# Kernel optimization log

Hardware: AMD Instinct MI355X
Metric: run time of the kernel (lower is better)

The kernel has to match this reference:

```python
import jax, jax.numpy as jnp
import numpy as np

B, CD, GD, F, H = 8192, 512, 512, 1024, 8
HD = F // H
EPS = 1e-5  # torch LayerNorm default


def _layernorm(x, g, b):
    m = x.mean(-1, keepdims=True)
    v = ((x - m) ** 2).mean(-1, keepdims=True)
    return (x - m) / jnp.sqrt(v + EPS) * g + b


def setup_inputs() -> dict:
    key = jax.random.key(0)
    ks = jax.random.split(key, 24)
    s = lambda fan_in: 1.0 / np.sqrt(fan_in)
    return {
        "cnn_embed": jax.random.normal(ks[0], (B, CD), jnp.float32),
        "gnn_embed": jax.random.normal(ks[1], (B, GD), jnp.float32),
        # projections (torch Linear: y = x @ W.T + b)
        "cnn_w": jax.random.normal(ks[2], (F, CD), jnp.float32) * s(CD),
        "cnn_b": jax.random.normal(ks[3], (F,), jnp.float32) * s(CD),
        "gnn_w": jax.random.normal(ks[4], (F, GD), jnp.float32) * s(GD),
        "gnn_b": jax.random.normal(ks[5], (F,), jnp.float32) * s(GD),
        # layernorms
        "ln1_g": jnp.ones((F,), jnp.float32),
        "ln1_b": jnp.zeros((F,), jnp.float32),
        "ln2_g": jnp.ones((F,), jnp.float32),
        "ln2_b": jnp.zeros((F,), jnp.float32),
        # MultiheadAttention packed in-proj + out-proj
        "attn_in_w": jax.random.normal(ks[6], (3 * F, F), jnp.float32) * s(F),
        "attn_in_b": jnp.zeros((3 * F,), jnp.float32),
        "attn_out_w": jax.random.normal(ks[7], (F, F), jnp.float32) * s(F),
        "attn_out_b": jnp.zeros((F,), jnp.float32),
        # gate MLP: Linear(2F->F) GELU Linear(F->2) Softmax
        "gate_w1": jax.random.normal(ks[8], (F, 2 * F), jnp.float32) * s(2 * F),
        "gate_b1": jnp.zeros((F,), jnp.float32),
        "gate_w2": jax.random.normal(ks[9], (2, F), jnp.float32) * s(F),
        "gate_b2": jnp.zeros((2,), jnp.float32),
        # out_proj: Linear(F->F) GELU (dropout is identity in eval)
        "proj_w": jax.random.normal(ks[10], (F, F), jnp.float32) * s(F),
        "proj_b": jnp.zeros((F,), jnp.float32),
    }


def reference(cnn_embed, gnn_embed, cnn_w, cnn_b, gnn_w, gnn_b,
              ln1_g, ln1_b, ln2_g, ln2_b,
              attn_in_w, attn_in_b, attn_out_w, attn_out_b,
              gate_w1, gate_b1, gate_w2, gate_b2, proj_w, proj_b):
    c = _layernorm(cnn_embed @ cnn_w.T + cnn_b, ln1_g, ln1_b)  # [B,F]
    g = _layernorm(gnn_embed @ gnn_w.T + gnn_b, ln2_g, ln2_b)  # [B,F]
    combined = jnp.stack([c, g], axis=1)  # [B,2,F]

    # self-attention over the 2-token "sequence" (q=k=v=combined)
    qkv = combined @ attn_in_w.T + attn_in_b  # [B,2,3F]
    q, k, v = jnp.split(qkv, 3, axis=-1)
    split_heads = lambda t: t.reshape(B, 2, H, HD).transpose(0, 2, 1, 3)  # [B,H,2,HD]
    q, k, v = split_heads(q), split_heads(k), split_heads(v)
    scores = jnp.einsum("bhqd,bhkd->bhqk", q, k) / np.sqrt(HD)  # [B,H,2,2]
    attn = jax.nn.softmax(scores, axis=-1)
    o = jnp.einsum("bhqk,bhkd->bhqd", attn, v)  # [B,H,2,HD]
    o = o.transpose(0, 2, 1, 3).reshape(B, 2, F)
    attn_out = o @ attn_out_w.T + attn_out_b  # [B,2,F]

    c_attn = attn_out[:, 0]
    g_attn = attn_out[:, 1]
    gate_in = jnp.concatenate([c_attn, g_attn], axis=-1)  # [B,2F]
    gate_h = jax.nn.gelu(gate_in @ gate_w1.T + gate_b1, approximate=False)
    gate_weights = jax.nn.softmax(gate_h @ gate_w2.T + gate_b2, axis=-1)  # [B,2]

    fused = gate_weights[:, 0:1] * c_attn + gate_weights[:, 1:2] * g_attn
    fused = jax.nn.gelu(fused @ proj_w.T + proj_b, approximate=False)  # dropout=eval identity
    return fused, gate_weights
```

## Files before the change

kernel.cpp:

```cpp
#include <hip/hip_runtime.h>
#include <hip/hip_bf16.h>
#include <math.h>

typedef short short8 __attribute__((ext_vector_type(8)));
typedef ushort ushort8v __attribute__((ext_vector_type(8)));
typedef float floatx4 __attribute__((ext_vector_type(4)));

__device__ __forceinline__ float bf2f(ushort u) {
    union { unsigned int i; float f; } v; v.i = ((unsigned int)u) << 16; return v.f;
}
__device__ __forceinline__ ushort f2bf(float f) {
    union { float f; unsigned int i; } v; v.f = f;
    unsigned int x = v.i;
    unsigned int lsb = (x >> 16) & 1u;
    x += 0x7fffu + lsb;
    return (ushort)(x >> 16);
}
__device__ __forceinline__ float gelu_f(float x) {
    return 0.5f * x * (1.0f + erff(x * 0.7071067811865475f));
}
__device__ __forceinline__ void store4(ushort* p, float a, float b, float c, float d) {
    ushort4 o; o.x = f2bf(a); o.y = f2bf(b); o.z = f2bf(c); o.w = f2bf(d);
    *(ushort4*)p = o;
}
__device__ __forceinline__ void store4(float* p, float a, float b, float c, float d) {
    *(float4*)p = make_float4(a, b, c, d);
}

struct CvtDesc {
    const float* in[6];
    ushort* out[6];
    int nblk[6];
};
__global__ __launch_bounds__(256) void cvt_all_kernel(CvtDesc d) {
    int b = blockIdx.x;
    int s = 0;
    int off = b;
    while (off >= d.nblk[s]) { off -= d.nblk[s]; s++; }
    int i = off * 1024 + threadIdx.x * 4;
    float4 v = *(const float4*)(d.in[s] + i);
    ushort4 o;
    o.x = f2bf(v.x); o.y = f2bf(v.y); o.z = f2bf(v.z); o.w = f2bf(v.w);
    *(ushort4*)(d.out[s] + i) = o;
}

template<int ACT, int AF32, typename TOUT>
__device__ __forceinline__ void gemm_core(const void* __restrict__ Av, int lda,
                                          const ushort* __restrict__ W,
                                          const float* __restrict__ bias,
                                          TOUT* __restrict__ C, int ldc,
                                          int K, int m0, int n0) {
    __shared__ ushort lsA[128 * 64];
    __shared__ ushort lsB[128 * 64];
    const int t = threadIdx.x;
    const int w = t >> 6, l = t & 63;
    const int q = l >> 4, r16 = l & 15;
    const int wm = (w >> 1) * 64, wn = (w & 1) * 64;

    floatx4 acc[4][4];
#pragma unroll
    for (int i = 0; i < 4; i++)
#pragma unroll
        for (int j = 0; j < 4; j++) acc[i][j] = (floatx4){0.f, 0.f, 0.f, 0.f};

    const int srow = t >> 3;
    const int lc   = t & 7;
    const int s7 = r16 & 7;
    const int e0 = ((q)     ^ s7) * 8;
    const int e1 = ((q + 4) ^ s7) * 8;

    for (int kt = 0; kt < K; kt += 64) {
        __syncthreads();
#pragma unroll
        for (int rr = 0; rr < 4; ++rr) {
            const int row = rr * 32 + srow;
            const int gc  = (lc ^ (row & 7)) * 8;
            const ushort* gb = W + (size_t)(n0 + row) * K + kt + gc;
            __builtin_amdgcn_global_load_lds((const __attribute__((address_space(1))) void*)gb,
                                             (__attribute__((address_space(3))) void*)&lsB[row * 64 + lc * 8],
                                             16, 0, 0);
            if (!AF32) {
                const ushort* ga = (const ushort*)Av + (size_t)(m0 + row) * lda + kt + gc;
                __builtin_amdgcn_global_load_lds((const __attribute__((address_space(1))) void*)ga,
                                                 (__attribute__((address_space(3))) void*)&lsA[row * 64 + lc * 8],
                                                 16, 0, 0);
            } else {
                const float* ga = (const float*)Av + (size_t)(m0 + row) * lda + kt + gc;
                float4 f0 = *(const float4*)ga;
                float4 f1 = *(const float4*)(ga + 4);
                ushort8v u;
                u[0] = f2bf(f0.x); u[1] = f2bf(f0.y); u[2] = f2bf(f0.z); u[3] = f2bf(f0.w);
                u[4] = f2bf(f1.x); u[5] = f2bf(f1.y); u[6] = f2bf(f1.z); u[7] = f2bf(f1.w);
                *(ushort8v*)&lsA[row * 64 + lc * 8] = u;
            }
        }
        __syncthreads();
        {
            short8 af[4], bfr[4];
#pragma unroll
            for (int i = 0; i < 4; i++) af[i]  = *(const short8*)&lsA[(wm + i * 16 + r16) * 64 + e0];
#pragma unroll
            for (int j = 0; j < 4; j++) bfr[j] = *(const short8*)&lsB[(wn + j * 16 + r16) * 64 + e0];
#pragma unroll
            for (int i = 0; i < 4; i++)
#pragma unroll
                for (int j = 0; j < 4; j++)
                    acc[i][j] = __builtin_amdgcn_mfma_f32_16x16x32_bf16(bfr[j], af[i], acc[i][j], 0, 0, 0);
#pragma unroll
            for (int i = 0; i < 4; i++) af[i]  = *(const short8*)&lsA[(wm + i * 16 + r16) * 64 + e1];
#pragma unroll
            for (int j = 0; j < 4; j++) bfr[j] = *(const short8*)&lsB[(wn + j * 16 + r16) * 64 + e1];
#pragma unroll
            for (int i = 0; i < 4; i++)
#pragma unroll
                for (int j = 0; j < 4; j++)
                    acc[i][j] = __builtin_amdgcn_mfma_f32_16x16x32_bf16(bfr[j], af[i], acc[i][j], 0, 0, 0);
        }
    }

#pragma unroll
    for (int j = 0; j < 4; j++) {
        const int col = n0 + wn + j * 16 + q * 4;
        const float4 bv = *(const float4*)(bias + col);
#pragma unroll
        for (int i = 0; i < 4; i++) {
            const int row = m0 + wm + i * 16 + r16;
            float v0 = acc[i][j][0] + bv.x;
            float v1 = acc[i][j][1] + bv.y;
            float v2 = acc[i][j][2] + bv.z;
            float v3 = acc[i][j][3] + bv.w;
            if (ACT == 1) { v0 = gelu_f(v0); v1 = gelu_f(v1); v2 = gelu_f(v2); v3 = gelu_f(v3); }
            store4(&C[(size_t)row * ldc + col], v0, v1, v2, v3);
        }
    }
}

template<int ACT, typename TOUT>
__global__ __launch_bounds__(256, 4) void gemm_bt(const ushort* __restrict__ A, int lda,
                                                  const ushort* __restrict__ W,
                                                  const float* __restrict__ bias,
                                                  TOUT* __restrict__ C, int ldc, int K) {
    gemm_core<ACT, 0, TOUT>(A, lda, W, bias, C, ldc, K, blockIdx.y * 128, blockIdx.x * 128);
}

__global__ __launch_bounds__(256, 3) void embed_gemm(const float* __restrict__ A0,
                                                     const float* __restrict__ A1,
                                                     const ushort* __restrict__ W0,
                                                     const ushort* __restrict__ W1,
                                                     const float* __restrict__ b0,
                                                     const float* __restrict__ b1,
                                                     ushort* __restrict__ C) {
    const int z = blockIdx.z;
    gemm_core<0, 1, ushort>(z ? (const void*)A1 : (const void*)A0, 512,
                            z ? W1 : W0, z ? b1 : b0,
                            C + z * 1024, 2048, 512,
                            blockIdx.y * 128, blockIdx.x * 128);
}

__global__ __launch_bounds__(256) void ln_kernel(ushort* __restrict__ comb,
                                                 const float* __restrict__ g1, const float* __restrict__ b1,
                                                 const float* __restrict__ g2, const float* __restrict__ b2) {
    int row = blockIdx.x;
    int s = row & 1;
    const float* g = s ? g2 : g1;
    const float* bb = s ? b2 : b1;
    ushort* p = comb + (size_t)row * 1024;
    int t = threadIdx.x;
    ushort4 u = *(const ushort4*)(p + t * 4);
    float x0 = bf2f(u.x), x1 = bf2f(u.y), x2 = bf2f(u.z), x3 = bf2f(u.w);
    float sum = x0 + x1 + x2 + x3;
    float ss = x0 * x0 + x1 * x1 + x2 * x2 + x3 * x3;
#pragma unroll
    for (int off = 32; off; off >>= 1) {
        sum += __shfl_xor(sum, off);
        ss  += __shfl_xor(ss, off);
    }
    __shared__ float sm[8];
    int wv = t >> 6, l = t & 63;
    if (l == 0) { sm[wv * 2] = sum; sm[wv * 2 + 1] = ss; }
    __syncthreads();
    sum = sm[0] + sm[2] + sm[4] + sm[6];
    ss  = sm[1] + sm[3] + sm[5] + sm[7];
    float mean = sum * (1.0f / 1024.0f);
    float var  = ss * (1.0f / 1024.0f) - mean * mean;
    float rstd = rsqrtf(var + 1e-5f);
    float4 gv = *(const float4*)(g + t * 4);
    float4 bv = *(const float4*)(bb + t * 4);
    ushort4 o;
    o.x = f2bf((x0 - mean) * rstd * gv.x + bv.x);
    o.y = f2bf((x1 - mean) * rstd * gv.y + bv.y);
    o.z = f2bf((x2 - mean) * rstd * gv.z + bv.z);
    o.w = f2bf((x3 - mean) * rstd * gv.w + bv.w);
    *(ushort4*)(p + t * 4) = o;
}

__global__ __launch_bounds__(256) void attn_kernel(const ushort* __restrict__ qkv,
                                                   ushort* __restrict__ O) {
    __shared__ ushort ls[6144];
    const int b = blockIdx.x;
    const int t = threadIdx.x;
    const ushort* src = qkv + (size_t)b * 6144;
#pragma unroll
    for (int p = 0; p < 3; ++p) {
        int idx = (p * 256 + t) * 8;
        *(ushort8v*)&ls[idx] = *(const ushort8v*)&src[idx];
    }
    __syncthreads();
    const int h = t >> 5, d32 = t & 31;
    const int o0 = h * 128 + d32 * 4;
    ushort4 uq0 = *(const ushort4*)&ls[o0];
    ushort4 uq1 = *(const ushort4*)&ls[3072 + o0];
    ushort4 uk0 = *(const ushort4*)&ls[1024 + o0];
    ushort4 uk1 = *(const ushort4*)&ls[4096 + o0];
    ushort4 uv0 = *(const ushort4*)&ls[2048 + o0];
    ushort4 uv1 = *(const ushort4*)&ls[5120 + o0];
    float q0[4] = {bf2f(uq0.x), bf2f(uq0.y), bf2f(uq0.z), bf2f(uq0.w)};
    float q1[4] = {bf2f(uq1.x), bf2f(uq1.y), bf2f(uq1.z), bf2f(uq1.w)};
    float k0[4] = {bf2f(uk0.x), bf2f(uk0.y), bf2f(uk0.z), bf2f(uk0.w)};
    float k1[4] = {bf2f(uk1.x), bf2f(uk1.y), bf2f(uk1.z), bf2f(uk1.w)};
    float v0[4] = {bf2f(uv0.x), bf2f(uv0.y), bf2f(uv0.z), bf2f(uv0.w)};
    float v1[4] = {bf2f(uv1.x), bf2f(uv1.y), bf2f(uv1.z), bf2f(uv1.w)};
    float p00 = 0.f, p01 = 0.f, p10 = 0.f, p11 = 0.f;
#pragma unroll
    for (int i = 0; i < 4; i++) {
        p00 += q0[i] * k0[i];
        p01 += q0[i] * k1[i];
        p10 += q1[i] * k0[i];
        p11 += q1[i] * k1[i];
    }
#pragma unroll
    for (int off = 16; off; off >>= 1) {
        p00 += __shfl_xor(p00, off);
        p01 += __shfl_xor(p01, off);
        p10 += __shfl_xor(p10, off);
        p11 += __shfl_xor(p11, off);
    }
    const float sc = 0.08838834764831845f;
    p00 *= sc; p01 *= sc; p10 *= sc; p11 *= sc;
    float m0 = fmaxf(p00, p01), m1 = fmaxf(p10, p11);
    float e00 = expf(p00 - m0), e01 = expf(p01 - m0);
    float e10 = expf(p10 - m1), e11 = expf(p11 - m1);
    float i0 = 1.0f / (e00 + e01), i1 = 1.0f / (e10 + e11);
    float a00 = e00 * i0, a01 = e01 * i0;
    float a10 = e10 * i1, a11 = e11 * i1;
    ushort* dst0 = O + (size_t)(b * 2) * 1024 + o0;
    ushort* dst1 = dst0 + 1024;
    store4(dst0, a00 * v0[0] + a01 * v1[0], a00 * v0[1] + a01 * v1[1],
                 a00 * v0[2] + a01 * v1[2], a00 * v0[3] + a01 * v1[3]);
    store4(dst1, a10 * v0[0] + a11 * v1[0], a10 * v0[1] + a11 * v1[1],
                 a10 * v0[2] + a11 * v1[2], a10 * v0[3] + a11 * v1[3]);
}

__global__ __launch_bounds__(256) void gate2_kernel(const ushort* __restrict__ gate_h,
                                                    const float* __restrict__ w2, const float* __restrict__ b2,
                                                    const ushort* __restrict__ attn_out,
                                                    ushort* __restrict__ fused_pre,
                                                    float* __restrict__ gw_out) {
    int b = blockIdx.x;
    int t = threadIdx.x;
    const ushort* hp = gate_h + (size_t)b * 1024;
    ushort4 u = *(const ushort4*)(hp + t * 4);
    float4 w0 = *(const float4*)(w2 + t * 4);
    float4 w1 = *(const float4*)(w2 + 1024 + t * 4);
    float h0 = bf2f(u.x), h1 = bf2f(u.y), h2 = bf2f(u.z), h3 = bf2f(u.w);
    float p0 = h0 * w0.x + h1 * w0.y + h2 * w0.z + h3 * w0.w;
    float p1 = h0 * w1.x + h1 * w1.y + h2 * w1.z + h3 * w1.w;
#pragma unroll
    for (int off = 32; off; off >>= 1) {
        p0 += __shfl_xor(p0, off);
        p1 += __shfl_xor(p1, off);
    }
    __shared__ float sm[8];
    __shared__ float sgw[2];
    int wv = t >> 6, l = t & 63;
    if (l == 0) { sm[wv * 2] = p0; sm[wv * 2 + 1] = p1; }
    __syncthreads();
    if (t == 0) {
        float d0 = sm[0] + sm[2] + sm[4] + sm[6] + b2[0];
        float d1 = sm[1] + sm[3] + sm[5] + sm[7] + b2[1];
        float mx = fmaxf(d0, d1);
        float e0 = expf(d0 - mx), e1 = expf(d1 - mx);
        float inv = 1.0f / (e0 + e1);
        sgw[0] = e0 * inv; sgw[1] = e1 * inv;
        gw_out[b * 2] = e0 * inv;
        gw_out[b * 2 + 1] = e1 * inv;
    }
    __syncthreads();
    float g0 = sgw[0], g1 = sgw[1];
    const ushort* ca = attn_out + (size_t)b * 2048;
    ushort* fp = fused_pre + (size_t)b * 1024;
    ushort4 uc = *(const ushort4*)(ca + t * 4);
    ushort4 ug = *(const ushort4*)(ca + 1024 + t * 4);
    ushort4 o;
    o.x = f2bf(g0 * bf2f(uc.x) + g1 * bf2f(ug.x));
    o.y = f2bf(g0 * bf2f(uc.y) + g1 * bf2f(ug.y));
    o.z = f2bf(g0 * bf2f(uc.z) + g1 * bf2f(ug.z));
    o.w = f2bf(g0 * bf2f(uc.w) + g1 * bf2f(ug.w));
    *(ushort4*)(fp + t * 4) = o;
}

#define OFF_W_CNN  16777216u
#define OFF_W_GNN  17825792u
#define OFF_W_QKV  18874368u
#define OFF_W_AO   25165824u
#define OFF_W_G1   27262976u
#define OFF_W_PJ   31457280u
#define OFF_COMB   33554432u
#define OFF_QKV    67108864u
#define OFF_AO     167772160u

extern "C" void kernel_launch(void* const* d_in, const int* in_sizes, int n_in,
                              void* d_out, int out_size, void* d_ws, size_t ws_size,
                              hipStream_t stream) {
    const float* cnn_embed  = (const float*)d_in[0];
    const float* gnn_embed  = (const float*)d_in[1];
    const float* cnn_w      = (const float*)d_in[2];
    const float* cnn_b      = (const float*)d_in[3];
    const float* gnn_w      = (const float*)d_in[4];
    const float* gnn_b      = (const float*)d_in[5];
    const float* ln1_g      = (const float*)d_in[6];
    const float* ln1_b      = (const float*)d_in[7];
    const float* ln2_g      = (const float*)d_in[8];
    const float* ln2_b      = (const float*)d_in[9];
    const float* attn_in_w  = (const float*)d_in[10];
    const float* attn_in_b  = (const float*)d_in[11];
    const float* attn_out_w = (const float*)d_in[12];
    const float* attn_out_b = (const float*)d_in[13];
    const float* gate_w1    = (const float*)d_in[14];
    const float* gate_b1    = (const float*)d_in[15];
    const float* gate_w2    = (const float*)d_in[16];
    const float* gate_b2    = (const float*)d_in[17];
    const float* proj_w     = (const float*)d_in[18];
    const float* proj_b     = (const float*)d_in[19];

    char* ws = (char*)d_ws;
    ushort* w_cnn  = (ushort*)(ws + OFF_W_CNN);
    ushort* w_gnn  = (ushort*)(ws + OFF_W_GNN);
    ushort* w_qkv  = (ushort*)(ws + OFF_W_QKV);
    ushort* w_ao   = (ushort*)(ws + OFF_W_AO);
    ushort* w_g1   = (ushort*)(ws + OFF_W_G1);
    ushort* w_pj   = (ushort*)(ws + OFF_W_PJ);
    ushort* comb   = (ushort*)(ws + OFF_COMB);
    ushort* qkv    = (ushort*)(ws + OFF_QKV);
    ushort* ao     = (ushort*)(ws + OFF_AO);
    ushort* Obuf      = (ushort*)(ws + OFF_COMB);
    ushort* gate_h    = (ushort*)(ws + OFF_COMB);
    ushort* fused_pre = (ushort*)(ws + OFF_COMB + 16777216u);

    float* out_f  = (float*)d_out;
    float* gw_out = out_f + 8192 * 1024;

    CvtDesc cd;
    cd.in[0] = cnn_w;      cd.out[0] = w_cnn; cd.nblk[0] = 512;
    cd.in[1] = gnn_w;      cd.out[1] = w_gnn; cd.nblk[1] = 512;
    cd.in[2] = attn_in_w;  cd.out[2] = w_qkv; cd.nblk[2] = 3072;
    cd.in[3] = attn_out_w; cd.out[3] = w_ao;  cd.nblk[3] = 1024;
    cd.in[4] = gate_w1;    cd.out[4] = w_g1;  cd.nblk[4] = 2048;
    cd.in[5] = proj_w;     cd.out[5] = w_pj;  cd.nblk[5] = 1024;
    cvt_all_kernel<<<8192, 256, 0, stream>>>(cd);

    dim3 blk(256);

    dim3 g_embed(1024 / 128, 8192 / 128, 2);
    embed_gemm<<<g_embed, blk, 0, stream>>>(cnn_embed, gnn_embed, w_cnn, w_gnn, cnn_b, gnn_b, comb);

    ln_kernel<<<16384, blk, 0, stream>>>(comb, ln1_g, ln1_b, ln2_g, ln2_b);

    dim3 g_qkv(3072 / 128, 16384 / 128);
    gemm_bt<0, ushort><<<g_qkv, blk, 0, stream>>>(comb, 1024, w_qkv, attn_in_b, qkv, 3072, 1024);

    attn_kernel<<<8192, blk, 0, stream>>>(qkv, Obuf);

    dim3 g_ao(1024 / 128, 16384 / 128);
    gemm_bt<0, ushort><<<g_ao, blk, 0, stream>>>(Obuf, 1024, w_ao, attn_out_b, ao, 1024, 1024);

    dim3 g_g1(1024 / 128, 8192 / 128);
    gemm_bt<1, ushort><<<g_g1, blk, 0, stream>>>(ao, 2048, w_g1, gate_b1, gate_h, 1024, 2048);

    gate2_kernel<<<8192, blk, 0, stream>>>(gate_h, gate_w2, gate_b2, ao, fused_pre, gw_out);

    dim3 g_pj(1024 / 128, 8192 / 128);
    gemm_bt<1, float><<<g_pj, blk, 0, stream>>>(fused_pre, 1024, w_pj, proj_b, out_f, 1024, 1024);
}
```

Before: 494.6 us.

## Fuse attention-weighted V and gated combine into GEMM A-operand staging

The attention kernel now only computes the 2x2 softmax weights per head. The weighted sum over V is computed on the fly while staging the A tile of the attention-output GEMM. Likewise the gate kernel only writes the gate weights, and the gated combine of c_attn and g_attn happens inside the projection GEMM's A staging. This removes two intermediate bf16 buffers and their round trips through global memory. The cost is that those GEMMs lose the async global-to-LDS DMA path for A and redo the combine arithmetic for every N-tile, with min-waves dropped to 3.

```diff
diff --git a/kernel.cpp b/kernel.cpp
--- a/kernel.cpp
+++ b/kernel.cpp
@@ -44,8 +44,62 @@
     *(ushort4*)(d.out[s] + i) = o;
 }
 
-template<int ACT, int AF32, typename TOUT>
-__device__ __forceinline__ void gemm_core(const void* __restrict__ Av, int lda,
+struct StageDMA {
+    const ushort* A; int lda;
+    __device__ __forceinline__ void stage(int row, int kof, ushort* dst) const {
+        const ushort* g = A + (size_t)row * lda + kof;
+        __builtin_amdgcn_global_load_lds((const __attribute__((address_space(1))) void*)g,
+                                         (__attribute__((address_space(3))) void*)dst,
+                                         16, 0, 0);
+    }
+};
+struct StageF32 {
+    const float* A; int lda;
+    __device__ __forceinline__ void stage(int row, int kof, ushort* dst) const {
+        const float* g = A + (size_t)row * lda + kof;
+        float4 f0 = *(const float4*)g;
+        float4 f1 = *(const float4*)(g + 4);
+        ushort8v u;
+        u[0] = f2bf(f0.x); u[1] = f2bf(f0.y); u[2] = f2bf(f0.z); u[3] = f2bf(f0.w);
+        u[4] = f2bf(f1.x); u[5] = f2bf(f1.y); u[6] = f2bf(f1.z); u[7] = f2bf(f1.w);
+        *(ushort8v*)dst = u;
+    }
+};
+struct StageAttnO {
+    const ushort* qkv;
+    const float4* aw;
+    __device__ __forceinline__ void stage(int row, int kof, ushort* dst) const {
+        const int p = row >> 1, m = row & 1;
+        const int h = kof >> 7, off = kof & 127;
+        const ushort* v0 = qkv + (size_t)(p * 2) * 3072 + 2048 + h * 128 + off;
+        ushort8v a = *(const ushort8v*)v0;
+        ushort8v b = *(const ushort8v*)(v0 + 3072);
+        float4 w4 = aw[p * 8 + h];
+        float w0 = m ? w4.z : w4.x;
+        float w1 = m ? w4.w : w4.y;
+        ushort8v u;
+#pragma unroll
+        for (int k = 0; k < 8; k++) u[k] = f2bf(w0 * bf2f(a[k]) + w1 * bf2f(b[k]));
+        *(ushort8v*)dst = u;
+    }
+};
+struct StageGComb {
+    const ushort* ao;
+    const float* gw;
+    __device__ __forceinline__ void stage(int row, int kof, ushort* dst) const {
+        const ushort* c = ao + (size_t)(row * 2) * 1024 + kof;
+        ushort8v a = *(const ushort8v*)c;
+        ushort8v b = *(const ushort8v*)(c + 1024);
+        float g0 = gw[row * 2], g1 = gw[row * 2 + 1];
+        ushort8v u;
+#pragma unroll
+        for (int k = 0; k < 8; k++) u[k] = f2bf(g0 * bf2f(a[k]) + g1 * bf2f(b[k]));
+        *(ushort8v*)dst = u;
+    }
+};
+
+template<int ACT, class StA, typename TOUT>
+__device__ __forceinline__ void gemm_core(StA sa,
                                           const ushort* __restrict__ W,
                                           const float* __restrict__ bias,
                                           TOUT* __restrict__ C, int ldc,
@@ -79,20 +133,7 @@
             __builtin_amdgcn_global_load_lds((const __attribute__((address_space(1))) void*)gb,
                                              (__attribute__((address_space(3))) void*)&lsB[row * 64 + lc * 8],
                                              16, 0, 0);
-            if (!AF32) {
-                const ushort* ga = (const ushort*)Av + (size_t)(m0 + row) * lda + kt + gc;
-                __builtin_amdgcn_global_load_lds((const __attribute__((address_space(1))) void*)ga,
-                                                 (__attribute__((address_space(3))) void*)&lsA[row * 64 + lc * 8],
-                                                 16, 0, 0);
-            } else {
-                const float* ga = (const float*)Av + (size_t)(m0 + row) * lda + kt + gc;
-                float4 f0 = *(const float4*)ga;
-                float4 f1 = *(const float4*)(ga + 4);
-                ushort8v u;
-                u[0] = f2bf(f0.x); u[1] = f2bf(f0.y); u[2] = f2bf(f0.z); u[3] = f2bf(f0.w);
-                u[4] = f2bf(f1.x); u[5] = f2bf(f1.y); u[6] = f2bf(f1.z); u[7] = f2bf(f1.w);
-                *(ushort8v*)&lsA[row * 64 + lc * 8] = u;
-            }
+            sa.stage(m0 + row, kt + gc, &lsA[row * 64 + lc * 8]);
         }
         __syncthreads();
         {
@@ -135,12 +176,12 @@
     }
 }
 
-template<int ACT, typename TOUT>
-__global__ __launch_bounds__(256, 4) void gemm_bt(const ushort* __restrict__ A, int lda,
-                                                  const ushort* __restrict__ W,
-                                                  const float* __restrict__ bias,
-                                                  TOUT* __restrict__ C, int ldc, int K) {
-    gemm_core<ACT, 0, TOUT>(A, lda, W, bias, C, ldc, K, blockIdx.y * 128, blockIdx.x * 128);
+template<int ACT, int MINW, class StA, typename TOUT>
+__global__ __launch_bounds__(256, MINW) void gemm_ker(StA sa,
+                                                      const ushort* __restrict__ W,
+                                                      const float* __restrict__ bias,
+                                                      TOUT* __restrict__ C, int ldc, int K) {
+    gemm_core<ACT, StA, TOUT>(sa, W, bias, C, ldc, K, blockIdx.y * 128, blockIdx.x * 128);
 }
 
 __global__ __launch_bounds__(256, 3) void embed_gemm(const float* __restrict__ A0,
@@ -151,10 +192,10 @@
                                                      const float* __restrict__ b1,
                                                      ushort* __restrict__ C) {
     const int z = blockIdx.z;
-    gemm_core<0, 1, ushort>(z ? (const void*)A1 : (const void*)A0, 512,
-                            z ? W1 : W0, z ? b1 : b0,
-                            C + z * 1024, 2048, 512,
-                            blockIdx.y * 128, blockIdx.x * 128);
+    StageF32 sa{z ? A1 : A0, 512};
+    gemm_core<0, StageF32, ushort>(sa, z ? W1 : W0, z ? b1 : b0,
+                                   C + z * 1024, 2048, 512,
+                                   blockIdx.y * 128, blockIdx.x * 128);
 }
 
 __global__ __launch_bounds__(256) void ln_kernel(ushort* __restrict__ comb,
@@ -194,32 +235,21 @@
     *(ushort4*)(p + t * 4) = o;
 }
 
-__global__ __launch_bounds__(256) void attn_kernel(const ushort* __restrict__ qkv,
-                                                   ushort* __restrict__ O) {
-    __shared__ ushort ls[6144];
-    const int b = blockIdx.x;
+__global__ __launch_bounds__(256) void attn_w_kernel(const ushort* __restrict__ qkv,
+                                                     float4* __restrict__ aw) {
+    const int p = blockIdx.x;
     const int t = threadIdx.x;
-    const ushort* src = qkv + (size_t)b * 6144;
-#pragma unroll
-    for (int p = 0; p < 3; ++p) {
-        int idx = (p * 256 + t) * 8;
-        *(ushort8v*)&ls[idx] = *(const ushort8v*)&src[idx];
-    }
-    __syncthreads();
-    const int h = t >> 5, d32 = t & 31;
-    const int o0 = h * 128 + d32 * 4;
-    ushort4 uq0 = *(const ushort4*)&ls[o0];
-    ushort4 uq1 = *(const ushort4*)&ls[3072 + o0];
-    ushort4 uk0 = *(const ushort4*)&ls[1024 + o0];
-    ushort4 uk1 = *(const ushort4*)&ls[4096 + o0];
-    ushort4 uv0 = *(const ushort4*)&ls[2048 + o0];
-    ushort4 uv1 = *(const ushort4*)&ls[5120 + o0];
+    const int h = t >> 5, d = (t & 31) * 4;
+    const ushort* base0 = qkv + (size_t)(p * 2) * 3072 + h * 128 + d;
+    const ushort* base1 = base0 + 3072;
+    ushort4 uq0 = *(const ushort4*)base0;
+    ushort4 uq1 = *(const ushort4*)base1;
+    ushort4 uk0 = *(const ushort4*)(base0 + 1024);
+    ushort4 uk1 = *(const ushort4*)(base1 + 1024);
     float q0[4] = {bf2f(uq0.x), bf2f(uq0.y), bf2f(uq0.z), bf2f(uq0.w)};
     float q1[4] = {bf2f(uq1.x), bf2f(uq1.y), bf2f(uq1.z), bf2f(uq1.w)};
     float k0[4] = {bf2f(uk0.x), bf2f(uk0.y), bf2f(uk0.z), bf2f(uk0.w)};
     float k1[4] = {bf2f(uk1.x), bf2f(uk1.y), bf2f(uk1.z), bf2f(uk1.w)};
-    float v0[4] = {bf2f(uv0.x), bf2f(uv0.y), bf2f(uv0.z), bf2f(uv0.w)};
-    float v1[4] = {bf2f(uv1.x), bf2f(uv1.y), bf2f(uv1.z), bf2f(uv1.w)};
     float p00 = 0.f, p01 = 0.f, p10 = 0.f, p11 = 0.f;
 #pragma unroll
     for (int i = 0; i < 4; i++) {
@@ -241,25 +271,17 @@
     float e00 = expf(p00 - m0), e01 = expf(p01 - m0);
     float e10 = expf(p10 - m1), e11 = expf(p11 - m1);
     float i0 = 1.0f / (e00 + e01), i1 = 1.0f / (e10 + e11);
-    float a00 = e00 * i0, a01 = e01 * i0;
-    float a10 = e10 * i1, a11 = e11 * i1;
-    ushort* dst0 = O + (size_t)(b * 2) * 1024 + o0;
-    ushort* dst1 = dst0 + 1024;
-    store4(dst0, a00 * v0[0] + a01 * v1[0], a00 * v0[1] + a01 * v1[1],
-                 a00 * v0[2] + a01 * v1[2], a00 * v0[3] + a01 * v1[3]);
-    store4(dst1, a10 * v0[0] + a11 * v1[0], a10 * v0[1] + a11 * v1[1],
-                 a10 * v0[2] + a11 * v1[2], a10 * v0[3] + a11 * v1[3]);
-}
-
-__global__ __launch_bounds__(256) void gate2_kernel(const ushort* __restrict__ gate_h,
-                                                    const float* __restrict__ w2, const float* __restrict__ b2,
-                                                    const ushort* __restrict__ attn_out,
-                                                    ushort* __restrict__ fused_pre,
-                                                    float* __restrict__ gw_out) {
+    if ((t & 31) == 0)
+        aw[p * 8 + h] = make_float4(e00 * i0, e01 * i0, e10 * i1, e11 * i1);
+}
+
+__global__ __launch_bounds__(256) void gate2w_kernel(const ushort* __restrict__ gate_h,
+                                                     const float* __restrict__ w2,
+                                                     const float* __restrict__ b2,
+                                                     float* __restrict__ gw_out) {
     int b = blockIdx.x;
     int t = threadIdx.x;
-    const ushort* hp = gate_h + (size_t)b * 1024;
-    ushort4 u = *(const ushort4*)(hp + t * 4);
+    ushort4 u = *(const ushort4*)(gate_h + (size_t)b * 1024 + t * 4);
     float4 w0 = *(const float4*)(w2 + t * 4);
     float4 w1 = *(const float4*)(w2 + 1024 + t * 4);
     float h0 = bf2f(u.x), h1 = bf2f(u.y), h2 = bf2f(u.z), h3 = bf2f(u.w);
@@ -271,7 +293,6 @@
         p1 += __shfl_xor(p1, off);
     }
     __shared__ float sm[8];
-    __shared__ float sgw[2];
     int wv = t >> 6, l = t & 63;
     if (l == 0) { sm[wv * 2] = p0; sm[wv * 2 + 1] = p1; }
     __syncthreads();
@@ -281,24 +302,12 @@
         float mx = fmaxf(d0, d1);
         float e0 = expf(d0 - mx), e1 = expf(d1 - mx);
         float inv = 1.0f / (e0 + e1);
-        sgw[0] = e0 * inv; sgw[1] = e1 * inv;
-        gw_out[b * 2] = e0 * inv;
+        gw_out[b * 2]     = e0 * inv;
         gw_out[b * 2 + 1] = e1 * inv;
     }
-    __syncthreads();
-    float g0 = sgw[0], g1 = sgw[1];
-    const ushort* ca = attn_out + (size_t)b * 2048;
-    ushort* fp = fused_pre + (size_t)b * 1024;
-    ushort4 uc = *(const ushort4*)(ca + t * 4);
-    ushort4 ug = *(const ushort4*)(ca + 1024 + t * 4);
-    ushort4 o;
-    o.x = f2bf(g0 * bf2f(uc.x) + g1 * bf2f(ug.x));
-    o.y = f2bf(g0 * bf2f(uc.y) + g1 * bf2f(ug.y));
-    o.z = f2bf(g0 * bf2f(uc.z) + g1 * bf2f(ug.z));
-    o.w = f2bf(g0 * bf2f(uc.w) + g1 * bf2f(ug.w));
-    *(ushort4*)(fp + t * 4) = o;
-}
-
+}
+
+#define OFF_AW     0u
 #define OFF_W_CNN  16777216u
 #define OFF_W_GNN  17825792u
 #define OFF_W_QKV  18874368u
@@ -334,6 +343,7 @@
     const float* proj_b     = (const float*)d_in[19];
 
     char* ws = (char*)d_ws;
+    float4* awbuf  = (float4*)(ws + OFF_AW);
     ushort* w_cnn  = (ushort*)(ws + OFF_W_CNN);
     ushort* w_gnn  = (ushort*)(ws + OFF_W_GNN);
     ushort* w_qkv  = (ushort*)(ws + OFF_W_QKV);
@@ -343,9 +353,7 @@
     ushort* comb   = (ushort*)(ws + OFF_COMB);
     ushort* qkv    = (ushort*)(ws + OFF_QKV);
     ushort* ao     = (ushort*)(ws + OFF_AO);
-    ushort* Obuf      = (ushort*)(ws + OFF_COMB);
-    ushort* gate_h    = (ushort*)(ws + OFF_COMB);
-    ushort* fused_pre = (ushort*)(ws + OFF_COMB + 16777216u);
+    ushort* gate_h = (ushort*)(ws + OFF_COMB);
 
     float* out_f  = (float*)d_out;
     float* gw_out = out_f + 8192 * 1024;
@@ -367,18 +375,22 @@
     ln_kernel<<<16384, blk, 0, stream>>>(comb, ln1_g, ln1_b, ln2_g, ln2_b);
 
     dim3 g_qkv(3072 / 128, 16384 / 128);
-    gemm_bt<0, ushort><<<g_qkv, blk, 0, stream>>>(comb, 1024, w_qkv, attn_in_b, qkv, 3072, 1024);
-
-    attn_kernel<<<8192, blk, 0, stream>>>(qkv, Obuf);
+    gemm_ker<0, 4, StageDMA, ushort><<<g_qkv, blk, 0, stream>>>(
+        StageDMA{comb, 1024}, w_qkv, attn_in_b, qkv, 3072, 1024);
+
+    attn_w_kernel<<<8192, blk, 0, stream>>>(qkv, awbuf);
 
     dim3 g_ao(1024 / 128, 16384 / 128);
-    gemm_bt<0, ushort><<<g_ao, blk, 0, stream>>>(Obuf, 1024, w_ao, attn_out_b, ao, 1024, 1024);
+    gemm_ker<0, 3, StageAttnO, ushort><<<g_ao, blk, 0, stream>>>(
+        StageAttnO{qkv, awbuf}, w_ao, attn_out_b, ao, 1024, 1024);
 
     dim3 g_g1(1024 / 128, 8192 / 128);
-    gemm_bt<1, ushort><<<g_g1, blk, 0, stream>>>(ao, 2048, w_g1, gate_b1, gate_h, 1024, 2048);
-
-    gate2_kernel<<<8192, blk, 0, stream>>>(gate_h, gate_w2, gate_b2, ao, fused_pre, gw_out);
+    gemm_ker<1, 4, StageDMA, ushort><<<g_g1, blk, 0, stream>>>(
+        StageDMA{ao, 2048}, w_g1, gate_b1, gate_h, 1024, 2048);
+
+    gate2w_kernel<<<8192, blk, 0, stream>>>(gate_h, gate_w2, gate_b2, gw_out);
 
     dim3 g_pj(1024 / 128, 8192 / 128);
-    gemm_bt<1, float><<<g_pj, blk, 0, stream>>>(fused_pre, 1024, w_pj, proj_b, out_f, 1024, 1024);
-}
+    gemm_ker<1, 3, StageGComb, float><<<g_pj, blk, 0, stream>>>(
+        StageGComb{ao, gw_out}, w_pj, proj_b, out_f, 1024, 1024);
+}
```

Result: slower. 559.4 us (+13.1%).

## Switch GEMM core from 16x16x32 to 32x32x16 bf16 MFMA tiles

Applied to the files above, without the earlier changes.

Each wave now computes its 64x64 sub-tile with four 32x32x16 MFMAs per k-step instead of sixteen 16x16x32 MFMAs. This reduces LDS fragment reads per MFMA and improves operand reuse. The LDS swizzle offsets and the epilogue store mapping are rewritten to match the 32x32 accumulator layout. Occupancy in launch bounds drops from 4 to 3 blocks, which may lower latency hiding.

```diff
diff --git a/kernel.cpp b/kernel.cpp
--- a/kernel.cpp
+++ b/kernel.cpp
@@ -4,7 +4,7 @@
 
 typedef short short8 __attribute__((ext_vector_type(8)));
 typedef ushort ushort8v __attribute__((ext_vector_type(8)));
-typedef float floatx4 __attribute__((ext_vector_type(4)));
+typedef float floatx16 __attribute__((ext_vector_type(16)));
 
 __device__ __forceinline__ float bf2f(ushort u) {
     union { unsigned int i; float f; } v; v.i = ((unsigned int)u) << 16; return v.f;
@@ -54,20 +54,23 @@
     __shared__ ushort lsB[128 * 64];
     const int t = threadIdx.x;
     const int w = t >> 6, l = t & 63;
-    const int q = l >> 4, r16 = l & 15;
+    const int r32 = l & 31, h = l >> 5;
     const int wm = (w >> 1) * 64, wn = (w & 1) * 64;
 
-    floatx4 acc[4][4];
-#pragma unroll
-    for (int i = 0; i < 4; i++)
-#pragma unroll
-        for (int j = 0; j < 4; j++) acc[i][j] = (floatx4){0.f, 0.f, 0.f, 0.f};
+    floatx16 acc[2][2];
+#pragma unroll
+    for (int i = 0; i < 2; i++)
+#pragma unroll
+        for (int j = 0; j < 2; j++)
+#pragma unroll
+            for (int e = 0; e < 16; e++) acc[i][j][e] = 0.f;
 
     const int srow = t >> 3;
     const int lc   = t & 7;
-    const int s7 = r16 & 7;
-    const int e0 = ((q)     ^ s7) * 8;
-    const int e1 = ((q + 4) ^ s7) * 8;
+    const int s7   = r32 & 7;
+    int eoff[4];
+#pragma unroll
+    for (int s = 0; s < 4; s++) eoff[s] = ((2 * s + h) ^ s7) * 8;
 
     for (int kt = 0; kt < K; kt += 64) {
         __syncthreads();
@@ -95,48 +98,41 @@
             }
         }
         __syncthreads();
-        {
-            short8 af[4], bfr[4];
-#pragma unroll
-            for (int i = 0; i < 4; i++) af[i]  = *(const short8*)&lsA[(wm + i * 16 + r16) * 64 + e0];
-#pragma unroll
-            for (int j = 0; j < 4; j++) bfr[j] = *(const short8*)&lsB[(wn + j * 16 + r16) * 64 + e0];
-#pragma unroll
-            for (int i = 0; i < 4; i++)
-#pragma unroll
-                for (int j = 0; j < 4; j++)
-                    acc[i][j] = __builtin_amdgcn_mfma_f32_16x16x32_bf16(bfr[j], af[i], acc[i][j], 0, 0, 0);
-#pragma unroll
-            for (int i = 0; i < 4; i++) af[i]  = *(const short8*)&lsA[(wm + i * 16 + r16) * 64 + e1];
-#pragma unroll
-            for (int j = 0; j < 4; j++) bfr[j] = *(const short8*)&lsB[(wn + j * 16 + r16) * 64 + e1];
-#pragma unroll
-            for (int i = 0; i < 4; i++)
-#pragma unroll
-                for (int j = 0; j < 4; j++)
-                    acc[i][j] = __builtin_amdgcn_mfma_f32_16x16x32_bf16(bfr[j], af[i], acc[i][j], 0, 0, 0);
+#pragma unroll
+        for (int s = 0; s < 4; s++) {
+            short8 a0 = *(const short8*)&lsA[(wm +      r32) * 64 + eoff[s]];
+            short8 a1 = *(const short8*)&lsA[(wm + 32 + r32) * 64 + eoff[s]];
+            short8 b0 = *(const short8*)&lsB[(wn +      r32) * 64 + eoff[s]];
+            short8 b1 = *(const short8*)&lsB[(wn + 32 + r32) * 64 + eoff[s]];
+            acc[0][0] = __builtin_amdgcn_mfma_f32_32x32x16_bf16(b0, a0, acc[0][0], 0, 0, 0);
+            acc[0][1] = __builtin_amdgcn_mfma_f32_32x32x16_bf16(b1, a0, acc[0][1], 0, 0, 0);
+            acc[1][0] = __builtin_amdgcn_mfma_f32_32x32x16_bf16(b0, a1, acc[1][0], 0, 0, 0);
+            acc[1][1] = __builtin_amdgcn_mfma_f32_32x32x16_bf16(b1, a1, acc[1][1], 0, 0, 0);
         }
     }
 
 #pragma unroll
-    for (int j = 0; j < 4; j++) {
-        const int col = n0 + wn + j * 16 + q * 4;
-        const float4 bv = *(const float4*)(bias + col);
-#pragma unroll
-        for (int i = 0; i < 4; i++) {
-            const int row = m0 + wm + i * 16 + r16;
-            float v0 = acc[i][j][0] + bv.x;
-            float v1 = acc[i][j][1] + bv.y;
-            float v2 = acc[i][j][2] + bv.z;
-            float v3 = acc[i][j][3] + bv.w;
-            if (ACT == 1) { v0 = gelu_f(v0); v1 = gelu_f(v1); v2 = gelu_f(v2); v3 = gelu_f(v3); }
-            store4(&C[(size_t)row * ldc + col], v0, v1, v2, v3);
+    for (int j = 0; j < 2; j++) {
+#pragma unroll
+        for (int g = 0; g < 4; g++) {
+            const int col = n0 + wn + j * 32 + g * 8 + h * 4;
+            const float4 bv = *(const float4*)(bias + col);
+#pragma unroll
+            for (int i = 0; i < 2; i++) {
+                const int row = m0 + wm + i * 32 + r32;
+                float v0 = acc[i][j][g * 4 + 0] + bv.x;
+                float v1 = acc[i][j][g * 4 + 1] + bv.y;
+                float v2 = acc[i][j][g * 4 + 2] + bv.z;
+                float v3 = acc[i][j][g * 4 + 3] + bv.w;
+                if (ACT == 1) { v0 = gelu_f(v0); v1 = gelu_f(v1); v2 = gelu_f(v2); v3 = gelu_f(v3); }
+                store4(&C[(size_t)row * ldc + col], v0, v1, v2, v3);
+            }
         }
     }
 }
 
 template<int ACT, typename TOUT>
-__global__ __launch_bounds__(256, 4) void gemm_bt(const ushort* __restrict__ A, int lda,
+__global__ __launch_bounds__(256, 3) void gemm_bt(const ushort* __restrict__ A, int lda,
                                                   const ushort* __restrict__ W,
                                                   const float* __restrict__ bias,
                                                   TOUT* __restrict__ C, int ldc, int K) {
```

Measured after the change: 501.3 us. About the same (+1.3%).
